# Kernel optimization log

Hardware: AMD Instinct MI355X
Metric: run time of the kernel (lower is better)

Reference implementation:

```python
import jax, jax.numpy as jnp
import numpy as np

EMBEDDING_DIM = 128
NEG = -1000.0


def setup_inputs() -> dict:
    key = jax.random.key(0)
    ks = jax.random.split(key, 7)
    B, S_src, S_tgt, D = 2, 4096, 512, EMBEDDING_DIM
    return {
        "input_embeddings": jax.random.normal(ks[0], (B, S_src, D), dtype=jnp.float32),
        "token_attention_masks_source": jax.random.randint(ks[1], (B, S_src), 0, 2, dtype=jnp.int32),
        "token_attention_masks_target": jax.random.randint(ks[2], (B, S_tgt), 0, 2, dtype=jnp.int32),
        "encoder_output_embedding": jax.random.normal(ks[3], (B, S_tgt, D), dtype=jnp.float32),
        "w_query": jax.random.uniform(ks[4], (D, D), dtype=jnp.float32),
        "w_key": jax.random.uniform(ks[5], (D, D), dtype=jnp.float32),
        "w_value": jax.random.uniform(ks[6], (D, D), dtype=jnp.float32),
    }


def reference(input_embeddings, token_attention_masks_source,
              token_attention_masks_target, encoder_output_embedding,
              w_query, w_key, w_value):
    # Encoder self-attention branch (attention_type='encoder'), num_heads=1.
    D = w_query.shape[0]
    q = jnp.einsum('bsd,de->bse', input_embeddings, w_query)   # [B,S,D]
    k = jnp.einsum('bsd,de->bse', input_embeddings, w_key)     # [B,S,D]
    v = jnp.einsum('bsd,de->bse', input_embeddings, w_value)   # [B,S,D]
    scores = jnp.einsum('bsd,btd->bst', q, k) / jnp.sqrt(jnp.float32(D))
    # Original adds mask along the QUERY axis: mask[B,S] -> unsqueeze(-1).
    add_mask = jnp.where(token_attention_masks_source == 0, NEG, 0.0).astype(scores.dtype)
    scores = scores + add_mask[:, :, None]
    probs = jax.nn.softmax(scores, axis=2)                      # softmax over keys
    out = jnp.einsum('bst,btd->bsd', probs, v)                  # [B,S,D]
    return out
```

## Files before the change

kernel.cpp:

```cpp
#include <hip/hip_runtime.h>
#include <hip/hip_bf16.h>

#define S_SRC 4096
#define DIM 128
#define BATCH 2
#define NSP 8
#define NQB 32
#define NQG 512
#define NWIN 8

typedef unsigned short u16;
typedef unsigned int u32;
typedef __bf16 bf16x8 __attribute__((ext_vector_type(8)));
typedef float f32x4 __attribute__((ext_vector_type(4)));
typedef u32 u32x4 __attribute__((ext_vector_type(4)));
typedef u16 u16x4 __attribute__((ext_vector_type(4)));

__device__ __forceinline__ __bf16 bf_hi(float x) { return (__bf16)x; }
__device__ __forceinline__ __bf16 bf_lo(float x, __bf16 h) { return (__bf16)(x - (float)h); }
__device__ __forceinline__ u16 bfu(__bf16 h) { return __builtin_bit_cast(u16, h); }
__device__ __forceinline__ u16 f2bu(float x) { return __builtin_bit_cast(u16, (__bf16)x); }
__device__ __forceinline__ float bu2f(u16 u) { return (float)__builtin_bit_cast(__bf16, u); }
__device__ __forceinline__ u32 pk2(float lo, float hi) {
  return (u32)f2bu(lo) | ((u32)f2bu(hi) << 16);
}
__device__ __forceinline__ void g2l16(const u16* src, u16* ldst) {
  __builtin_amdgcn_global_load_lds((const __attribute__((address_space(1))) void*)src,
                                   (__attribute__((address_space(3))) void*)ldst, 16, 0, 0);
}
#define MFMA __builtin_amdgcn_mfma_f32_16x16x32_bf16

__global__ __launch_bounds__(256) void k_wsplit(const float* __restrict__ wq,
                                                const float* __restrict__ wk,
                                                const float* __restrict__ wv,
                                                u16* __restrict__ wt) {
  int idx = blockIdx.x * 256 + threadIdx.x;
  int mat = idx >> 14;
  int r = idx & 16383;
  int d = r >> 7, e = r & 127;
  const float* w = (mat == 0) ? wq : ((mat == 1) ? wk : wv);
  float x = w[r];
  if (mat == 0) x *= 0.08838834764831845f;
  __bf16 h = bf_hi(x);
  __bf16 l = bf_lo(x, h);
  wt[((mat * 2 + 0) * 128 + e) * 128 + d] = bfu(h);
  wt[((mat * 2 + 1) * 128 + e) * 128 + d] = bfu(l);
}

__global__ __launch_bounds__(256) void k_proj(const float* __restrict__ X,
                                              const u16* __restrict__ wt,
                                              u16* __restrict__ Qh, u16* __restrict__ Ql,
                                              u16* __restrict__ Kh, u16* __restrict__ Kl,
                                              u16* __restrict__ VT) {
  const int mat = blockIdx.x >> 8;
  const int t = blockIdx.x & 255;
  const int b = t >> 7;
  const int tile = t & 127;
  const int tid = threadIdx.x;
  const int w = tid >> 6, lane = tid & 63, g = lane >> 4, l16 = lane & 15;

  bf16x8 a_h[2][4], a_l[2][4];
#pragma unroll
  for (int mf = 0; mf < 2; ++mf) {
    int row = tile * 32 + mf * 16 + l16;
    const float* xr = X + ((size_t)b * S_SRC + row) * DIM;
#pragma unroll
    for (int kf = 0; kf < 4; ++kf) {
      int d0 = kf * 32 + g * 8;
      f32x4 x0 = *(const f32x4*)(xr + d0);
      f32x4 x1 = *(const f32x4*)(xr + d0 + 4);
#pragma unroll
      for (int j = 0; j < 4; ++j) {
        __bf16 h0 = bf_hi(x0[j]);
        __bf16 h1 = bf_hi(x1[j]);
        a_h[mf][kf][j] = h0;
        a_l[mf][kf][j] = bf_lo(x0[j], h0);
        a_h[mf][kf][4 + j] = h1;
        a_l[mf][kf][4 + j] = bf_lo(x1[j], h1);
      }
    }
  }

  const u16* wth = wt + (mat * 2 + 0) * 16384;
  const u16* wtl = wt + (mat * 2 + 1) * 16384;
#pragma unroll
  for (int nf = 0; nf < 2; ++nf) {
    int col = w * 32 + nf * 16 + l16;
    f32x4 acc[2];
    acc[0] = (f32x4){0.f, 0.f, 0.f, 0.f};
    acc[1] = (f32x4){0.f, 0.f, 0.f, 0.f};
#pragma unroll
    for (int kf = 0; kf < 4; ++kf) {
      int d0 = kf * 32 + g * 8;
      bf16x8 bh = *(const bf16x8*)(const void*)(wth + col * 128 + d0);
      bf16x8 bl = *(const bf16x8*)(const void*)(wtl + col * 128 + d0);
#pragma unroll
      for (int mf = 0; mf < 2; ++mf) {
        acc[mf] = MFMA(a_h[mf][kf], bh, acc[mf], 0, 0, 0);
        acc[mf] = MFMA(a_h[mf][kf], bl, acc[mf], 0, 0, 0);
        acc[mf] = MFMA(a_l[mf][kf], bh, acc[mf], 0, 0, 0);
      }
    }
#pragma unroll
    for (int mf = 0; mf < 2; ++mf)
#pragma unroll
      for (int r = 0; r < 4; ++r) {
        int row = tile * 32 + mf * 16 + g * 4 + r;
        float v = acc[mf][r];
        if (mat == 2) {
          VT[((size_t)b * DIM + col) * S_SRC + row] = f2bu(v);
        } else {
          __bf16 h = bf_hi(v);
          __bf16 l = bf_lo(v, h);
          size_t o = ((size_t)b * S_SRC + row) * DIM + col;
          if (mat == 0) { Qh[o] = bfu(h); Ql[o] = bfu(l); }
          else          { Kh[o] = bfu(h); Kl[o] = bfu(l); }
        }
      }
  }
}

__global__ __launch_bounds__(512, 2) void k_attn(const u16* __restrict__ Qh, const u16* __restrict__ Ql,
                                                 const u16* __restrict__ Kh, const u16* __restrict__ Kl,
                                                 const u16* __restrict__ VT,
                                                 float* __restrict__ Pm, float* __restrict__ Pl,
                                                 u16* __restrict__ PO) {
  const int bid = blockIdx.x;
  const int sp = bid & 7;
  const int qb = bid >> 3;
  const int b = qb >> 4;
  const int tid = threadIdx.x;
  const int w = tid >> 6, lane = tid & 63, g = lane >> 4, l16 = lane & 15;

  __shared__ alignas(16) u16 kbuf[3][16384];
  __shared__ alignas(16) u16 vbuf[3][8192];

  const int gr0 = qb * 256 + w * 32;
  bf16x8 qh0[4], ql0[4], qh1[4], ql1[4];
  {
    const u16* p0h = Qh + ((size_t)gr0 + l16) * DIM;
    const u16* p0l = Ql + ((size_t)gr0 + l16) * DIM;
    const u16* p1h = Qh + ((size_t)gr0 + 16 + l16) * DIM;
    const u16* p1l = Ql + ((size_t)gr0 + 16 + l16) * DIM;
#pragma unroll
    for (int kf = 0; kf < 4; ++kf) {
      int d0 = kf * 32 + g * 8;
      qh0[kf] = *(const bf16x8*)(const void*)(p0h + d0);
      ql0[kf] = *(const bf16x8*)(const void*)(p0l + d0);
      qh1[kf] = *(const bf16x8*)(const void*)(p1h + d0);
      ql1[kf] = *(const bf16x8*)(const void*)(p1l + d0);
    }
  }

  f32x4 acc0[8], acc1[8];
#pragma unroll
  for (int nf = 0; nf < 8; ++nf) {
    acc0[nf] = (f32x4){0.f, 0.f, 0.f, 0.f};
    acc1[nf] = (f32x4){0.f, 0.f, 0.f, 0.f};
  }
  float m0 = -1e30f, m1 = -1e30f, l0 = 0.f, l1 = 0.f;

  const int key_base = sp * (S_SRC / NSP);
  const u16* KhB = Kh + (size_t)b * S_SRC * DIM;
  const u16* KlB = Kl + (size_t)b * S_SRC * DIM;
  const u16* VTB = VT + (size_t)b * DIM * S_SRC;

  const int kkey0 = tid >> 4;
  const int kks = ((tid & 15) ^ (kkey0 & 15)) << 3;
  const int vd0 = tid >> 3;
  const int vks = ((tid & 7) ^ ((vd0 >> 1) & 7)) << 3;
  const int wb = w * 512;
  const int mg = ((g & 1) << 1) | (g >> 1);

#define STAGE(BUF, KEY0)                                                             \
  {                                                                                  \
    g2l16(KhB + ((size_t)((KEY0) + kkey0)) * DIM + kks,      &kbuf[BUF][wb]);        \
    g2l16(KhB + ((size_t)((KEY0) + 32 + kkey0)) * DIM + kks, &kbuf[BUF][4096 + wb]); \
    g2l16(KlB + ((size_t)((KEY0) + kkey0)) * DIM + kks,      &kbuf[BUF][8192 + wb]); \
    g2l16(KlB + ((size_t)((KEY0) + 32 + kkey0)) * DIM + kks, &kbuf[BUF][12288 + wb]);\
    g2l16(VTB + (size_t)vd0 * S_SRC + (KEY0) + vks,          &vbuf[BUF][wb]);        \
    g2l16(VTB + (size_t)(64 + vd0) * S_SRC + (KEY0) + vks,   &vbuf[BUF][4096 + wb]); \
  }

#define SMPACK(S, MR, LR, ACC, PA, PB)                                               \
  {                                                                                  \
    float mxa = fmaxf(fmaxf(fmaxf(S[0][0], S[0][1]), fmaxf(S[0][2], S[0][3])),       \
                      fmaxf(fmaxf(S[1][0], S[1][1]), fmaxf(S[1][2], S[1][3])));      \
    float mxb = fmaxf(fmaxf(fmaxf(S[2][0], S[2][1]), fmaxf(S[2][2], S[2][3])),       \
                      fmaxf(fmaxf(S[3][0], S[3][1]), fmaxf(S[3][2], S[3][3])));      \
    float mx = fmaxf(mxa, mxb);                                                      \
    mx = fmaxf(mx, __shfl_xor(mx, 16, 64));                                          \
    mx = fmaxf(mx, __shfl_xor(mx, 32, 64));                                          \
    if (!__all(mx - MR <= 8.0f)) {                                                   \
      float mn = fmaxf(MR, mx);                                                      \
      float f = __expf(MR - mn);                                                     \
      LR *= f; MR = mn;                                                              \
      float fr0 = __shfl(f, g * 4 + 0, 64);                                          \
      float fr1 = __shfl(f, g * 4 + 1, 64);                                          \
      float fr2 = __shfl(f, g * 4 + 2, 64);                                          \
      float fr3 = __shfl(f, g * 4 + 3, 64);                                          \
      _Pragma("unroll")                                                              \
      for (int nf = 0; nf < 8; ++nf) {                                               \
        ACC[nf][0] *= fr0; ACC[nf][1] *= fr1;                                        \
        ACC[nf][2] *= fr2; ACC[nf][3] *= fr3;                                        \
      }                                                                              \
    }                                                                                \
    float e0 = __expf(S[0][0] - MR), e1 = __expf(S[0][1] - MR);                      \
    float e2 = __expf(S[0][2] - MR), e3 = __expf(S[0][3] - MR);                      \
    float e4 = __expf(S[1][0] - MR), e5 = __expf(S[1][1] - MR);                      \
    float e6 = __expf(S[1][2] - MR), e7 = __expf(S[1][3] - MR);                      \
    float f0 = __expf(S[2][0] - MR), f1 = __expf(S[2][1] - MR);                      \
    float f2 = __expf(S[2][2] - MR), f3 = __expf(S[2][3] - MR);                      \
    float f4 = __expf(S[3][0] - MR), f5 = __expf(S[3][1] - MR);                      \
    float f6 = __expf(S[3][2] - MR), f7 = __expf(S[3][3] - MR);                      \
    float sm = (((e0 + e1) + (e2 + e3)) + ((e4 + e5) + (e6 + e7)))                   \
             + (((f0 + f1) + (f2 + f3)) + ((f4 + f5) + (f6 + f7)));                  \
    sm += __shfl_xor(sm, 16, 64);                                                    \
    sm += __shfl_xor(sm, 32, 64);                                                    \
    LR += sm;                                                                        \
    bool odd = (g & 1);                                                              \
    {                                                                                \
      u32 w0 = pk2(e0, e1), w1 = pk2(e2, e3), w2 = pk2(e4, e5), w3 = pk2(e6, e7);    \
      u32 x0 = __shfl_xor(w0, 16, 64), x1 = __shfl_xor(w1, 16, 64);                  \
      u32 x2 = __shfl_xor(w2, 16, 64), x3 = __shfl_xor(w3, 16, 64);                  \
      u32x4 pw;                                                                      \
      pw.x = odd ? x2 : w0; pw.y = odd ? x3 : w1;                                    \
      pw.z = odd ? w2 : x0; pw.w = odd ? w3 : x1;                                    \
      PA = __builtin_bit_cast(bf16x8, pw);                                           \
    }                                                                                \
    {                                                                                \
      u32 w0 = pk2(f0, f1), w1 = pk2(f2, f3), w2 = pk2(f4, f5), w3 = pk2(f6, f7);    \
      u32 x0 = __shfl_xor(w0, 16, 64), x1 = __shfl_xor(w1, 16, 64);                  \
      u32 x2 = __shfl_xor(w2, 16, 64), x3 = __shfl_xor(w3, 16, 64);                  \
      u32x4 pw;                                                                      \
      pw.x = odd ? x2 : w0; pw.y = odd ? x3 : w1;                                    \
      pw.z = odd ? w2 : x0; pw.w = odd ? w3 : x1;                                    \
      PB = __builtin_bit_cast(bf16x8, pw);                                           \
    }                                                                                \
  }

  STAGE(0, key_base)
  STAGE(1, key_base + 64)

  int cur = 0;
  for (int i = 0; i < NWIN; ++i) {
    if (i < NWIN - 1) {
      asm volatile("s_waitcnt vmcnt(6)" ::: "memory");
    } else {
      asm volatile("s_waitcnt vmcnt(0)" ::: "memory");
    }
    __builtin_amdgcn_s_barrier();
    if (i + 2 < NWIN) {
      int nx = cur + 2; nx = (nx >= 3) ? nx - 3 : nx;
      STAGE(nx, key_base + (i + 2) * 64)
    }

    const u16* kb = kbuf[cur];
    const u16* vb = vbuf[cur];

    f32x4 sg0[4], sg1[4];
#pragma unroll
    for (int st = 0; st < 4; ++st) {
      sg0[st] = (f32x4){0.f, 0.f, 0.f, 0.f};
      sg1[st] = (f32x4){0.f, 0.f, 0.f, 0.f};
    }
    __builtin_amdgcn_s_setprio(1);
#pragma unroll
    for (int kf = 0; kf < 4; ++kf) {
      int cs = ((kf * 4 + g) ^ l16) << 3;
#pragma unroll
      for (int st = 0; st < 4; ++st) {
        const u16* kp = kb + (st * 16 + l16) * 128 + cs;
        bf16x8 kh = *(const bf16x8*)(const void*)kp;
        bf16x8 kl = *(const bf16x8*)(const void*)(kp + 8192);
        sg0[st] = MFMA(kh, qh0[kf], sg0[st], 0, 0, 0);
        sg0[st] = MFMA(kh, ql0[kf], sg0[st], 0, 0, 0);
        sg0[st] = MFMA(kl, qh0[kf], sg0[st], 0, 0, 0);
        sg1[st] = MFMA(kh, qh1[kf], sg1[st], 0, 0, 0);
        sg1[st] = MFMA(kh, ql1[kf], sg1[st], 0, 0, 0);
        sg1[st] = MFMA(kl, qh1[kf], sg1[st], 0, 0, 0);
      }
    }
    __builtin_amdgcn_s_setprio(0);

    bf16x8 pa0A, pa0B, pa1A, pa1B;
    SMPACK(sg0, m0, l0, acc0, pa0A, pa0B)
    SMPACK(sg1, m1, l1, acc1, pa1A, pa1B)

    __builtin_amdgcn_s_setprio(1);
#pragma unroll
    for (int nf = 0; nf < 8; ++nf) {
      int d = nf * 16 + l16;
      int sw = (d >> 1) & 7;
      const u16* vr = vb + d * 64;
      bf16x8 vf0 = *(const bf16x8*)(const void*)(vr + ((mg ^ sw) << 3));
      bf16x8 vf1 = *(const bf16x8*)(const void*)(vr + (((4 + mg) ^ sw) << 3));
      acc0[nf] = MFMA(pa0A, vf0, acc0[nf], 0, 0, 0);
      acc0[nf] = MFMA(pa0B, vf1, acc0[nf], 0, 0, 0);
      acc1[nf] = MFMA(pa1A, vf0, acc1[nf], 0, 0, 0);
      acc1[nf] = MFMA(pa1B, vf1, acc1[nf], 0, 0, 0);
    }
    __builtin_amdgcn_s_setprio(0);

    cur = (cur + 1 >= 3) ? cur - 2 : cur + 1;
  }

  const int pidx0 = sp * NQG + (gr0 >> 4);
  {
    u16* po = PO + (size_t)pidx0 * 16 * DIM;
#pragma unroll
    for (int nf = 0; nf < 8; ++nf)
#pragma unroll
      for (int r = 0; r < 4; ++r)
        po[(g * 4 + r) * DIM + nf * 16 + l16] = f2bu(acc0[nf][r]);
    u16* po1 = PO + (size_t)(pidx0 + 1) * 16 * DIM;
#pragma unroll
    for (int nf = 0; nf < 8; ++nf)
#pragma unroll
      for (int r = 0; r < 4; ++r)
        po1[(g * 4 + r) * DIM + nf * 16 + l16] = f2bu(acc1[nf][r]);
  }
  if (g == 0) { Pm[pidx0 * 16 + l16] = m0; Pl[pidx0 * 16 + l16] = l0; }
  if (g == 1) { Pm[(pidx0 + 1) * 16 + l16] = m1; Pl[(pidx0 + 1) * 16 + l16] = l1; }
#undef STAGE
#undef SMPACK
}

__global__ __launch_bounds__(64) void k_comb(const float* __restrict__ Pm,
                                             const float* __restrict__ Pl,
                                             const u16* __restrict__ PO,
                                             float* __restrict__ out) {
  const int qg = blockIdx.x;
  const int tid = threadIdx.x;

  __shared__ float sc[NSP][16];
  if (tid < 16) {
    float m = -1e30f;
#pragma unroll
    for (int s = 0; s < NSP; ++s) m = fmaxf(m, Pm[(s * NQG + qg) * 16 + tid]);
    float den = 0.f;
#pragma unroll
    for (int s = 0; s < NSP; ++s) {
      float e = __expf(Pm[(s * NQG + qg) * 16 + tid] - m);
      sc[s][tid] = e;
      den += Pl[(s * NQG + qg) * 16 + tid] * e;
    }
    float inv = 1.0f / den;
#pragma unroll
    for (int s = 0; s < NSP; ++s) sc[s][tid] *= inv;
  }
  __syncthreads();

  float* op = out + (size_t)qg * 16 * DIM;
  for (int i = tid; i < 16 * DIM / 4; i += 64) {
    int row = (i * 4) >> 7;
    f32x4 a = (f32x4){0.f, 0.f, 0.f, 0.f};
#pragma unroll
    for (int s = 0; s < NSP; ++s) {
      u16x4 p = *(const u16x4*)(const void*)(PO + (size_t)(s * NQG + qg) * 16 * DIM + i * 4);
      float wgt = sc[s][row];
      a[0] += bu2f(p.x) * wgt;
      a[1] += bu2f(p.y) * wgt;
      a[2] += bu2f(p.z) * wgt;
      a[3] += bu2f(p.w) * wgt;
    }
    *(f32x4*)(op + i * 4) = a;
  }
}

extern "C" void kernel_launch(void* const* d_in, const int* in_sizes, int n_in,
                              void* d_out, int out_size, void* d_ws, size_t ws_size,
                              hipStream_t stream) {
  const float* X  = (const float*)d_in[0];
  const float* wq = (const float*)d_in[4];
  const float* wk = (const float*)d_in[5];
  const float* wv = (const float*)d_in[6];
  float* out = (float*)d_out;

  u16* WT = (u16*)d_ws;
  u16* Qh = WT + 3 * 2 * 128 * 128;
  u16* Ql = Qh + (size_t)BATCH * S_SRC * DIM;
  u16* Kh = Ql + (size_t)BATCH * S_SRC * DIM;
  u16* Kl = Kh + (size_t)BATCH * S_SRC * DIM;
  u16* VT = Kl + (size_t)BATCH * S_SRC * DIM;
  float* Pm = (float*)(VT + (size_t)BATCH * S_SRC * DIM);
  float* Pl = Pm + (size_t)NSP * NQG * 16;
  u16* PO = (u16*)(Pl + (size_t)NSP * NQG * 16);

  hipLaunchKernelGGL(k_wsplit, dim3(192), dim3(256), 0, stream, wq, wk, wv, WT);
  hipLaunchKernelGGL(k_proj, dim3(3 * 256), dim3(256), 0, stream,
                     X, WT, Qh, Ql, Kh, Kl, VT);
  hipLaunchKernelGGL(k_attn, dim3(NQB * NSP), dim3(512), 0, stream,
                     Qh, Ql, Kh, Kl, VT, Pm, Pl, PO);
  hipLaunchKernelGGL(k_comb, dim3(NQG), dim3(64), 0, stream, Pm, Pl, PO, out);
}
```

Baseline: 72.54 us.

## Fuse QKV projections per tile, use exp2 softmax, widen combine kernel

The projection kernel now loads and bf16-splits each X tile once and computes Q, K and V in a single block instead of three separate blocks, cutting redundant X reads and conversion work. The Q scale folds in log2(e), so the softmax uses exp2f directly, and the rescale threshold is raised to match the base-2 range. The combine kernel uses 256 threads, each handling eight contiguous elements with 16-byte loads, replacing the strided loop. The trade-offs are fewer projection blocks, more registers per block, and exp2 precision in the softmax.

```diff
diff --git a/kernel.cpp b/kernel.cpp
--- a/kernel.cpp
+++ b/kernel.cpp
@@ -14,7 +14,7 @@
 typedef __bf16 bf16x8 __attribute__((ext_vector_type(8)));
 typedef float f32x4 __attribute__((ext_vector_type(4)));
 typedef u32 u32x4 __attribute__((ext_vector_type(4)));
-typedef u16 u16x4 __attribute__((ext_vector_type(4)));
+typedef u16 u16x8 __attribute__((ext_vector_type(8)));
 
 __device__ __forceinline__ __bf16 bf_hi(float x) { return (__bf16)x; }
 __device__ __forceinline__ __bf16 bf_lo(float x, __bf16 h) { return (__bf16)(x - (float)h); }
@@ -40,7 +40,7 @@
   int d = r >> 7, e = r & 127;
   const float* w = (mat == 0) ? wq : ((mat == 1) ? wk : wv);
   float x = w[r];
-  if (mat == 0) x *= 0.08838834764831845f;
+  if (mat == 0) x *= 0.12751744684693238f;
   __bf16 h = bf_hi(x);
   __bf16 l = bf_lo(x, h);
   wt[((mat * 2 + 0) * 128 + e) * 128 + d] = bfu(h);
@@ -52,10 +52,8 @@
                                               u16* __restrict__ Qh, u16* __restrict__ Ql,
                                               u16* __restrict__ Kh, u16* __restrict__ Kl,
                                               u16* __restrict__ VT) {
-  const int mat = blockIdx.x >> 8;
-  const int t = blockIdx.x & 255;
-  const int b = t >> 7;
-  const int tile = t & 127;
+  const int b = blockIdx.x >> 7;
+  const int tile = blockIdx.x & 127;
   const int tid = threadIdx.x;
   const int w = tid >> 6, lane = tid & 63, g = lane >> 4, l16 = lane & 15;
 
@@ -81,42 +79,45 @@
     }
   }
 
-  const u16* wth = wt + (mat * 2 + 0) * 16384;
-  const u16* wtl = wt + (mat * 2 + 1) * 16384;
-#pragma unroll
-  for (int nf = 0; nf < 2; ++nf) {
-    int col = w * 32 + nf * 16 + l16;
-    f32x4 acc[2];
-    acc[0] = (f32x4){0.f, 0.f, 0.f, 0.f};
-    acc[1] = (f32x4){0.f, 0.f, 0.f, 0.f};
-#pragma unroll
-    for (int kf = 0; kf < 4; ++kf) {
-      int d0 = kf * 32 + g * 8;
-      bf16x8 bh = *(const bf16x8*)(const void*)(wth + col * 128 + d0);
-      bf16x8 bl = *(const bf16x8*)(const void*)(wtl + col * 128 + d0);
-#pragma unroll
-      for (int mf = 0; mf < 2; ++mf) {
-        acc[mf] = MFMA(a_h[mf][kf], bh, acc[mf], 0, 0, 0);
-        acc[mf] = MFMA(a_h[mf][kf], bl, acc[mf], 0, 0, 0);
-        acc[mf] = MFMA(a_l[mf][kf], bh, acc[mf], 0, 0, 0);
-      }
-    }
-#pragma unroll
-    for (int mf = 0; mf < 2; ++mf)
-#pragma unroll
-      for (int r = 0; r < 4; ++r) {
-        int row = tile * 32 + mf * 16 + g * 4 + r;
-        float v = acc[mf][r];
-        if (mat == 2) {
-          VT[((size_t)b * DIM + col) * S_SRC + row] = f2bu(v);
-        } else {
-          __bf16 h = bf_hi(v);
-          __bf16 l = bf_lo(v, h);
-          size_t o = ((size_t)b * S_SRC + row) * DIM + col;
-          if (mat == 0) { Qh[o] = bfu(h); Ql[o] = bfu(l); }
-          else          { Kh[o] = bfu(h); Kl[o] = bfu(l); }
+#pragma unroll
+  for (int mat = 0; mat < 3; ++mat) {
+    const u16* wth = wt + (mat * 2 + 0) * 16384;
+    const u16* wtl = wt + (mat * 2 + 1) * 16384;
+#pragma unroll
+    for (int nf = 0; nf < 2; ++nf) {
+      int col = w * 32 + nf * 16 + l16;
+      f32x4 acc[2];
+      acc[0] = (f32x4){0.f, 0.f, 0.f, 0.f};
+      acc[1] = (f32x4){0.f, 0.f, 0.f, 0.f};
+#pragma unroll
+      for (int kf = 0; kf < 4; ++kf) {
+        int d0 = kf * 32 + g * 8;
+        bf16x8 bh = *(const bf16x8*)(const void*)(wth + col * 128 + d0);
+        bf16x8 bl = *(const bf16x8*)(const void*)(wtl + col * 128 + d0);
+#pragma unroll
+        for (int mf = 0; mf < 2; ++mf) {
+          acc[mf] = MFMA(a_h[mf][kf], bh, acc[mf], 0, 0, 0);
+          acc[mf] = MFMA(a_h[mf][kf], bl, acc[mf], 0, 0, 0);
+          acc[mf] = MFMA(a_l[mf][kf], bh, acc[mf], 0, 0, 0);
         }
       }
+#pragma unroll
+      for (int mf = 0; mf < 2; ++mf)
+#pragma unroll
+        for (int r = 0; r < 4; ++r) {
+          int row = tile * 32 + mf * 16 + g * 4 + r;
+          float v = acc[mf][r];
+          if (mat == 2) {
+            VT[((size_t)b * DIM + col) * S_SRC + row] = f2bu(v);
+          } else {
+            __bf16 h = bf_hi(v);
+            __bf16 l = bf_lo(v, h);
+            size_t o = ((size_t)b * S_SRC + row) * DIM + col;
+            if (mat == 0) { Qh[o] = bfu(h); Ql[o] = bfu(l); }
+            else          { Kh[o] = bfu(h); Kl[o] = bfu(l); }
+          }
+        }
+    }
   }
 }
 
@@ -191,9 +192,9 @@
     float mx = fmaxf(mxa, mxb);                                                      \
     mx = fmaxf(mx, __shfl_xor(mx, 16, 64));                                          \
     mx = fmaxf(mx, __shfl_xor(mx, 32, 64));                                          \
-    if (!__all(mx - MR <= 8.0f)) {                                                   \
+    if (!__all(mx - MR <= 11.5f)) {                                                  \
       float mn = fmaxf(MR, mx);                                                      \
-      float f = __expf(MR - mn);                                                     \
+      float f = exp2f(MR - mn);                                                      \
       LR *= f; MR = mn;                                                              \
       float fr0 = __shfl(f, g * 4 + 0, 64);                                          \
       float fr1 = __shfl(f, g * 4 + 1, 64);                                          \
@@ -205,14 +206,14 @@
         ACC[nf][2] *= fr2; ACC[nf][3] *= fr3;                                        \
       }                                                                              \
     }                                                                                \
-    float e0 = __expf(S[0][0] - MR), e1 = __expf(S[0][1] - MR);                      \
-    float e2 = __expf(S[0][2] - MR), e3 = __expf(S[0][3] - MR);                      \
-    float e4 = __expf(S[1][0] - MR), e5 = __expf(S[1][1] - MR);                      \
-    float e6 = __expf(S[1][2] - MR), e7 = __expf(S[1][3] - MR);                      \
-    float f0 = __expf(S[2][0] - MR), f1 = __expf(S[2][1] - MR);                      \
-    float f2 = __expf(S[2][2] - MR), f3 = __expf(S[2][3] - MR);                      \
-    float f4 = __expf(S[3][0] - MR), f5 = __expf(S[3][1] - MR);                      \
-    float f6 = __expf(S[3][2] - MR), f7 = __expf(S[3][3] - MR);                      \
+    float e0 = exp2f(S[0][0] - MR), e1 = exp2f(S[0][1] - MR);                        \
+    float e2 = exp2f(S[0][2] - MR), e3 = exp2f(S[0][3] - MR);                        \
+    float e4 = exp2f(S[1][0] - MR), e5 = exp2f(S[1][1] - MR);                        \
+    float e6 = exp2f(S[1][2] - MR), e7 = exp2f(S[1][3] - MR);                        \
+    float f0 = exp2f(S[2][0] - MR), f1 = exp2f(S[2][1] - MR);                        \
+    float f2 = exp2f(S[2][2] - MR), f3 = exp2f(S[2][3] - MR);                        \
+    float f4 = exp2f(S[3][0] - MR), f5 = exp2f(S[3][1] - MR);                        \
+    float f6 = exp2f(S[3][2] - MR), f7 = exp2f(S[3][3] - MR);                        \
     float sm = (((e0 + e1) + (e2 + e3)) + ((e4 + e5) + (e6 + e7)))                   \
              + (((f0 + f1) + (f2 + f3)) + ((f4 + f5) + (f6 + f7)));                  \
     sm += __shfl_xor(sm, 16, 64);                                                    \
@@ -326,10 +327,10 @@
 #undef SMPACK
 }
 
-__global__ __launch_bounds__(64) void k_comb(const float* __restrict__ Pm,
-                                             const float* __restrict__ Pl,
-                                             const u16* __restrict__ PO,
-                                             float* __restrict__ out) {
+__global__ __launch_bounds__(256) void k_comb(const float* __restrict__ Pm,
+                                              const float* __restrict__ Pl,
+                                              const u16* __restrict__ PO,
+                                              float* __restrict__ out) {
   const int qg = blockIdx.x;
   const int tid = threadIdx.x;
 
@@ -341,7 +342,7 @@
     float den = 0.f;
 #pragma unroll
     for (int s = 0; s < NSP; ++s) {
-      float e = __expf(Pm[(s * NQG + qg) * 16 + tid] - m);
+      float e = exp2f(Pm[(s * NQG + qg) * 16 + tid] - m);
       sc[s][tid] = e;
       den += Pl[(s * NQG + qg) * 16 + tid] * e;
     }
@@ -351,21 +352,23 @@
   }
   __syncthreads();
 
-  float* op = out + (size_t)qg * 16 * DIM;
-  for (int i = tid; i < 16 * DIM / 4; i += 64) {
-    int row = (i * 4) >> 7;
-    f32x4 a = (f32x4){0.f, 0.f, 0.f, 0.f};
-#pragma unroll
-    for (int s = 0; s < NSP; ++s) {
-      u16x4 p = *(const u16x4*)(const void*)(PO + (size_t)(s * NQG + qg) * 16 * DIM + i * 4);
-      float wgt = sc[s][row];
-      a[0] += bu2f(p.x) * wgt;
-      a[1] += bu2f(p.y) * wgt;
-      a[2] += bu2f(p.z) * wgt;
-      a[3] += bu2f(p.w) * wgt;
-    }
-    *(f32x4*)(op + i * 4) = a;
-  }
+  const int e0 = tid * 8;
+  const int row = e0 >> 7;
+  float a[8];
+#pragma unroll
+  for (int j = 0; j < 8; ++j) a[j] = 0.f;
+#pragma unroll
+  for (int s = 0; s < NSP; ++s) {
+    u16x8 p = *(const u16x8*)(const void*)(PO + (size_t)(s * NQG + qg) * 16 * DIM + e0);
+    float wgt = sc[s][row];
+#pragma unroll
+    for (int j = 0; j < 8; ++j) a[j] += bu2f(p[j]) * wgt;
+  }
+  float* op = out + (size_t)qg * 16 * DIM + e0;
+  f32x4 o0 = {a[0], a[1], a[2], a[3]};
+  f32x4 o1 = {a[4], a[5], a[6], a[7]};
+  *(f32x4*)op = o0;
+  *(f32x4*)(op + 4) = o1;
 }
 
 extern "C" void kernel_launch(void* const* d_in, const int* in_sizes, int n_in,
@@ -388,9 +391,9 @@
   u16* PO = (u16*)(Pl + (size_t)NSP * NQG * 16);
 
   hipLaunchKernelGGL(k_wsplit, dim3(192), dim3(256), 0, stream, wq, wk, wv, WT);
-  hipLaunchKernelGGL(k_proj, dim3(3 * 256), dim3(256), 0, stream,
+  hipLaunchKernelGGL(k_proj, dim3(BATCH * S_SRC / 32), dim3(256), 0, stream,
                      X, WT, Qh, Ql, Kh, Kl, VT);
   hipLaunchKernelGGL(k_attn, dim3(NQB * NSP), dim3(512), 0, stream,
                      Qh, Ql, Kh, Kl, VT, Pm, Pl, PO);
-  hipLaunchKernelGGL(k_comb, dim3(NQG), dim3(64), 0, stream, Pm, Pl, PO, out);
-}
+  hipLaunchKernelGGL(k_comb, dim3(NQG), dim3(256), 0, stream, Pm, Pl, PO, out);
+}
```

Measured after the change: 72.23 us. About the same (-0.4%).
